# Optimization experiments

Hardware: AMD Instinct MI355X
Metric: run time of the kernel (lower is better)

## Reference

```python
import jax, jax.numpy as jnp
import numpy as np

N_NODES = 100000
N_CLIQUES = 50000
N_EDGES = 1600000
D_IN = 128
D_OUT = 128


def setup_inputs() -> dict:
    key = jax.random.key(0)
    k1, k2, k3, k4, k5, k6 = jax.random.split(key, 6)
    x = jax.random.normal(k1, (N_NODES, D_IN), dtype=jnp.float32)
    x_clique = jax.random.normal(k2, (N_CLIQUES, D_IN), dtype=jnp.float32)
    node_idx = jax.random.randint(k3, (N_EDGES,), 0, N_NODES, dtype=jnp.int64)
    clique_idx = jax.random.randint(k4, (N_EDGES,), 0, N_CLIQUES, dtype=jnp.int64)
    node2clique_index = jnp.stack([node_idx, clique_idx], axis=0)
    # Linear(in, out): weight [out, in], bias [out]
    W = jax.random.normal(k5, (D_OUT, D_IN), dtype=jnp.float32) * (1.0 / np.sqrt(D_IN))
    b = jax.random.normal(k6, (D_OUT,), dtype=jnp.float32) * 0.01
    return {"x": x, "x_clique": x_clique, "node2clique_index": node2clique_index, "W": W, "b": b}


def reference(x, x_clique, node2clique_index, W, b):
    node_idx = node2clique_index[0]
    clique_idx = node2clique_index[1]
    n_nodes = x.shape[0]
    gathered = x_clique[clique_idx]                                   # [E, D_in]
    summed = jax.ops.segment_sum(gathered, node_idx, num_segments=n_nodes)  # [N, D_in]
    count = jax.ops.segment_sum(
        jnp.ones((gathered.shape[0],), dtype=x_clique.dtype), node_idx, num_segments=n_nodes
    )
    mean = summed / jnp.maximum(count, 1.0)[:, None]                  # scatter-mean, count clamped like torch_scatter
    out = mean @ W.T + b                                              # Linear
    return out
```

## Files before the change

kernel.cpp:

```cpp
#include <hip/hip_runtime.h>


typedef short bf16x8 __attribute__((ext_vector_type(8)));
typedef float f32x4  __attribute__((ext_vector_type(4)));
typedef float f32x2  __attribute__((ext_vector_type(2)));

#define BK_SHIFT 8
#define NB_MAX 512
#define BCUR_STRIDE 16
#define RAWCAP 4608
#define PADCAP 6400
#define FCHUNK 4096

__device__ inline ushort f2b(float f) {
    union { float f; uint u; } v; v.f = f;
    uint r = v.u + 0x7FFFu + ((v.u >> 16) & 1u);
    return (ushort)(r >> 16);
}
__device__ inline float blo(uint v) { union { uint u; float f; } x; x.u = v << 16;        return x.f; }
__device__ inline float bhi(uint v) { union { uint u; float f; } x; x.u = v & 0xFFFF0000u; return x.f; }

struct FillSM {
    int cnt[NB_MAX];
    int sloc[NB_MAX];
    int gbase[NB_MAX];
    int cur[NB_MAX];
    int wtot[8];
    uint   stage[FCHUNK];
    ushort sbkt[FCHUNK];
};
struct TransSM { ushort wl[128 * 128]; };

__global__ __launch_bounds__(512) void k_front(const float* __restrict__ xc,
                                               const float* __restrict__ W,
                                               ushort* __restrict__ yb, int nc,
                                               const int* __restrict__ nidx,
                                               const int* __restrict__ cidx,
                                               int* __restrict__ bcur,
                                               uint* __restrict__ pairs,
                                               int ne, int gf) {
    __shared__ union USM { FillSM f; TransSM tr; } sm;
    const int t = threadIdx.x;
    const int lane = t & 63, wid = t >> 6;

    if ((int)blockIdx.x < gf) {
        const int e0 = blockIdx.x * FCHUNK;
        const int e1 = min(e0 + FCHUNK, ne);
        sm.f.cnt[t] = 0;
        sm.f.cur[t] = 0;
        __syncthreads();

        int nn[8], cc[8];
        #pragma unroll
        for (int k = 0; k < 8; ++k) {
            int i = e0 + k * 512 + t;
            if (i < e1) {
                nn[k] = nidx[i];
                cc[k] = cidx[i];
                atomicAdd(&sm.f.cnt[nn[k] >> BK_SHIFT], 1);
            } else nn[k] = -1;
        }
        __syncthreads();

        int v = sm.f.cnt[t];
        int inc = v;
        #pragma unroll
        for (int d = 1; d < 64; d <<= 1) { int x = __shfl_up(inc, d); if (lane >= d) inc += x; }
        if (lane == 63) sm.f.wtot[wid] = inc;
        __syncthreads();
        int wpre = 0;
        for (int i = 0; i < wid; ++i) wpre += sm.f.wtot[i];
        int excl = wpre + inc - v;
        sm.f.sloc[t] = excl;
        if (v > 0) sm.f.gbase[t] = t * RAWCAP + atomicAdd(&bcur[t * BCUR_STRIDE], v);
        __syncthreads();

        #pragma unroll
        for (int k = 0; k < 8; ++k) {
            if (nn[k] >= 0) {
                int b = nn[k] >> BK_SHIFT;
                int slot = sm.f.sloc[b] + atomicAdd(&sm.f.cur[b], 1);
                sm.f.stage[slot] = ((uint)(nn[k] & 255) << 16) | (uint)cc[k];
                sm.f.sbkt[slot] = (ushort)b;
            }
        }
        __syncthreads();

        const int m = e1 - e0;
        for (int i = t; i < m; i += 512) {
            int b = sm.f.sbkt[i];
            pairs[(size_t)sm.f.gbase[b] + (i - sm.f.sloc[b])] = sm.f.stage[i];
        }
    } else {
        const int bid = blockIdx.x - gf;
        if (bid == 0 && t < 64)
            reinterpret_cast<uint*>(&yb[(size_t)nc * 128])[t] = 0u;
        for (int i = 0; i < 8; ++i) {
            int idx = (i * 512 + t) * 4;
            float4 w4 = *reinterpret_cast<const float4*>(&W[idx]);
            int o = idx >> 7, k = idx & 127;
            ushort4 h;
            h.x = f2b(w4.x); h.y = f2b(w4.y); h.z = f2b(w4.z); h.w = f2b(w4.w);
            int byte = o * 256 + k * 2;
            byte ^= (o & 7) << 4;
            *reinterpret_cast<ushort4*>(reinterpret_cast<char*>(sm.tr.wl) + byte) = h;
        }
        __syncthreads();

        const int lrow = lane & 15;
        const int lk = lane >> 4;
        const int r0 = bid * 128 + wid * 16;
        const bool rowok = (r0 + lrow) < nc;
        const float* arow = &xc[(size_t)(r0 + lrow) * 128];

        bf16x8 afrag[4];
        for (int kb = 0; kb < 4; ++kb) {
            float4 a0 = make_float4(0.f, 0.f, 0.f, 0.f), a1 = a0;
            if (rowok) {
                int k0 = kb * 32 + lk * 8;
                a0 = *reinterpret_cast<const float4*>(&arow[k0]);
                a1 = *reinterpret_cast<const float4*>(&arow[k0 + 4]);
            }
            bf16x8 a;
            a[0] = (short)f2b(a0.x); a[1] = (short)f2b(a0.y);
            a[2] = (short)f2b(a0.z); a[3] = (short)f2b(a0.w);
            a[4] = (short)f2b(a1.x); a[5] = (short)f2b(a1.y);
            a[6] = (short)f2b(a1.z); a[7] = (short)f2b(a1.w);
            afrag[kb] = a;
        }

        for (int ct = 0; ct < 8; ++ct) {
            f32x4 c = {0.f, 0.f, 0.f, 0.f};
            const int o = ct * 16 + lrow;
            #pragma unroll
            for (int kb = 0; kb < 4; ++kb) {
                int byte = o * 256 + (kb * 32 + lk * 8) * 2;
                byte ^= (o & 7) << 4;
                bf16x8 bb = *reinterpret_cast<const bf16x8*>(reinterpret_cast<const char*>(sm.tr.wl) + byte);
                c = __builtin_amdgcn_mfma_f32_16x16x32_bf16(afrag[kb], bb, c, 0, 0, 0);
            }
            const int orow = r0 + lk * 4;
            #pragma unroll
            for (int j = 0; j < 4; ++j)
                if (orow + j < nc)
                    yb[(size_t)(orow + j) * 128 + ct * 16 + lrow] = f2b(c[j]);
        }
    }
}

__global__ __launch_bounds__(512) void k_build(const uint* __restrict__ pairs,
                                               const int* __restrict__ bcur,
                                               int* __restrict__ offsets,
                                               int* __restrict__ ncnt,
                                               ushort* __restrict__ edge_dst,
                                               int n_nodes, int nc) {
    __shared__ int arr[256], nexcl[256], cur[256], wtot[4];
    __shared__ int mpad_sh;
    __shared__ ushort scidx[PADCAP];
    const int b = blockIdx.x, t = threadIdx.x;
    const int p0r = b * RAWCAP;
    const int p0e = b * PADCAP;
    const int m = min(bcur[b * BCUR_STRIDE], RAWCAP);
    const int node0 = b << BK_SHIFT;

    if (t < 256) { arr[t] = 0; cur[t] = 0; }
    __syncthreads();
    for (int i = t; i < m; i += 512)
        atomicAdd(&arr[pairs[p0r + i] >> 16], 1);
    __syncthreads();

    int v = 0, pv = 0, inc = 0;
    if (t < 256) {
        v = arr[t];
        pv = (v + 7) & ~7;
        inc = pv;
        #pragma unroll
        for (int d = 1; d < 64; d <<= 1) {
            int x = __shfl_up(inc, d);
            if ((t & 63) >= d) inc += x;
        }
        if ((t & 63) == 63) wtot[t >> 6] = inc;
    }
    __syncthreads();
    if (t < 256) {
        const int wid = t >> 6;
        int wpre = 0;
        for (int i = 0; i < wid; ++i) wpre += wtot[i];
        const int excl = wpre + inc - pv;
        nexcl[t] = excl;
        if (node0 + t < n_nodes) {
            offsets[node0 + t] = p0e + excl;
            ncnt[node0 + t] = v;
        }
        if (t == 255) mpad_sh = excl + pv;
    }
    __syncthreads();

    for (int i = t; i < m; i += 512) {
        uint p = pairs[p0r + i];
        int l = (int)(p >> 16);
        int slot = nexcl[l] + atomicAdd(&cur[l], 1);
        scidx[slot] = (ushort)(p & 0xFFFFu);
    }
    __syncthreads();
    if (t < 256) {
        const int base = nexcl[t];
        for (int k = v; k < pv; ++k)
            scidx[base + k] = (ushort)nc;
    }
    __syncthreads();
    const int mp2 = mpad_sh >> 1;
    uint* ed32 = reinterpret_cast<uint*>(edge_dst);
    const uint* sc32 = reinterpret_cast<const uint*>(scidx);
    const int p0e2 = p0e >> 1;
    for (int i = t; i < mp2; i += 512)
        ed32[p0e2 + i] = sc32[i];
}

__global__ __launch_bounds__(256) void k_reduce(const ushort* __restrict__ yb,
                                                const int* __restrict__ offsets,
                                                const int* __restrict__ ncnt,
                                                const ushort* __restrict__ edge_dst,
                                                const float* __restrict__ bias,
                                                float* __restrict__ out, int n) {
    int w = (blockIdx.x * blockDim.x + threadIdx.x) >> 6;
    int nA = w << 1;
    if (nA >= n) return;
    const int lane = threadIdx.x & 63;
    const int nAu = __builtin_amdgcn_readfirstlane(nA);
    const int sA = offsets[nAu];
    const int cA = ncnt[nAu];
    const bool hasB = (nAu + 1) < n;
    const int sB = hasB ? offsets[nAu + 1] : sA;
    const int cB = hasB ? ncnt[nAu + 1] : 0;
    const int eA = (cA + 7) & ~7;
    const int eB = (cB + 7) & ~7;
    const char* ybase = reinterpret_cast<const char*>(yb) + lane * 4;

    float axA0 = 0.f, ayA0 = 0.f, axA1 = 0.f, ayA1 = 0.f;
    float axB0 = 0.f, ayB0 = 0.f, axB1 = 0.f, ayB1 = 0.f;
    const int rounds = (max(eA, eB) + 7) >> 3;
    for (int r = 0; r < rounds; ++r) {
        const int j = r << 3;
        const bool doA = j < eA, doB = j < eB;
        uint vA[8], vB[8];
        if (doA) {
            #pragma unroll
            for (int u = 0; u < 8; ++u) {
                int c = edge_dst[sA + j + u];
                vA[u] = *reinterpret_cast<const uint*>(ybase + (size_t)c * 256);
            }
        }
        if (doB) {
            #pragma unroll
            for (int u = 0; u < 8; ++u) {
                int c = edge_dst[sB + j + u];
                vB[u] = *reinterpret_cast<const uint*>(ybase + (size_t)c * 256);
            }
        }
        if (doA) {
            #pragma unroll
            for (int u = 0; u < 8; u += 2) {
                axA0 += blo(vA[u]);     ayA0 += bhi(vA[u]);
                axA1 += blo(vA[u + 1]); ayA1 += bhi(vA[u + 1]);
            }
        }
        if (doB) {
            #pragma unroll
            for (int u = 0; u < 8; u += 2) {
                axB0 += blo(vB[u]);     ayB0 += bhi(vB[u]);
                axB1 += blo(vB[u + 1]); ayB1 += bhi(vB[u + 1]);
            }
        }
    }
    const f32x2 bv = *reinterpret_cast<const f32x2*>(&bias[lane * 2]);
    {
        float ax = axA0 + axA1, ay = ayA0 + ayA1;
        float inv = 1.0f / (float)max(cA, 1);
        f32x2 o;
        o.x = ax * inv + bv.x;
        o.y = ay * inv + bv.y;
        __builtin_nontemporal_store(o, reinterpret_cast<f32x2*>(&out[(size_t)nA * 128 + lane * 2]));
    }
    if (hasB) {
        float ax = axB0 + axB1, ay = ayB0 + ayB1;
        float inv = 1.0f / (float)max(cB, 1);
        f32x2 o;
        o.x = ax * inv + bv.x;
        o.y = ay * inv + bv.y;
        __builtin_nontemporal_store(o, reinterpret_cast<f32x2*>(&out[((size_t)nA + 1) * 128 + lane * 2]));
    }
}

extern "C" void kernel_launch(void* const* d_in, const int* in_sizes, int n_in,
                              void* d_out, int out_size, void* d_ws, size_t ws_size,
                              hipStream_t stream) {
    const float* xc  = (const float*)d_in[1];
    const int*   n2c = (const int*)d_in[2];
    const float* W   = (const float*)d_in[3];
    const float* b   = (const float*)d_in[4];
    float* out = (float*)d_out;

    const int n_nodes   = in_sizes[0] / 128;
    const int n_cliques = in_sizes[1] / 128;
    const int n_edges   = in_sizes[2] / 2;
    const int* nidx = n2c;
    const int* cidx = n2c + n_edges;
    const int nbucket = (n_nodes + ((1 << BK_SHIFT) - 1)) >> BK_SHIFT;

    char* ws = (char*)d_ws;
    size_t off = 0;
    ushort* yb = (ushort*)(ws + off);     off += (size_t)(n_cliques + 1) * 128 * sizeof(ushort);
    off = (off + 15) & ~(size_t)15;
    uint* pairs = (uint*)(ws + off);      off += (size_t)nbucket * RAWCAP * sizeof(uint);
    ushort* edge_dst = (ushort*)(ws + off); off += (size_t)nbucket * PADCAP * sizeof(ushort);
    off = (off + 15) & ~(size_t)15;
    int* offsets = (int*)(ws + off);      off += (size_t)n_nodes * sizeof(int);
    int* ncnt = (int*)(ws + off);         off += (size_t)n_nodes * sizeof(int);
    int* bcur = (int*)(ws + off);         off += (size_t)NB_MAX * BCUR_STRIDE * sizeof(int);

    (void)hipMemsetAsync(bcur, 0, (size_t)NB_MAX * BCUR_STRIDE * sizeof(int), stream);

    const int gf = (n_edges + FCHUNK - 1) / FCHUNK;
    const int gt = (n_cliques + 127) / 128;
    k_front<<<gf + gt, 512, 0, stream>>>(xc, W, yb, n_cliques, nidx, cidx, bcur,
                                         pairs, n_edges, gf);
    k_build<<<nbucket, 512, 0, stream>>>(pairs, bcur, offsets, ncnt, edge_dst,
                                         n_nodes, n_cliques);
    const int nwaves = (n_nodes + 1) / 2;
    k_reduce<<<(nwaves * 64 + 255) / 256, 256, 0, stream>>>(yb, offsets, ncnt, edge_dst, b, out, n_nodes);
}
```

Baseline: 96.27 us.

## Reduce one node per wave with 16-byte gathers across four edge groups

The reduce kernel now gives each wave one node instead of two. The wave is split into four groups of 16 lanes; each group handles every fourth edge and each lane gathers 16 bytes (8 bf16 values) of a projected clique row. Partial sums are combined with cross-lane shuffles, and only 16 lanes write the output row. This aims for wider gather loads and more edges in flight per wave, at the cost of shuffle reductions and idle lanes during the final write. Separately, the transform blocks in the front kernel each process 256 clique rows instead of 128, so the W load into shared memory is spread over more rows.

```diff
diff --git a/kernel.cpp b/kernel.cpp
--- a/kernel.cpp
+++ b/kernel.cpp
@@ -109,41 +109,43 @@
 
         const int lrow = lane & 15;
         const int lk = lane >> 4;
-        const int r0 = bid * 128 + wid * 16;
-        const bool rowok = (r0 + lrow) < nc;
-        const float* arow = &xc[(size_t)(r0 + lrow) * 128];
-
-        bf16x8 afrag[4];
-        for (int kb = 0; kb < 4; ++kb) {
-            float4 a0 = make_float4(0.f, 0.f, 0.f, 0.f), a1 = a0;
-            if (rowok) {
-                int k0 = kb * 32 + lk * 8;
-                a0 = *reinterpret_cast<const float4*>(&arow[k0]);
-                a1 = *reinterpret_cast<const float4*>(&arow[k0 + 4]);
+        for (int g = 0; g < 2; ++g) {
+            const int r0 = bid * 256 + g * 128 + wid * 16;
+            const bool rowok = (r0 + lrow) < nc;
+            const float* arow = &xc[(size_t)(r0 + lrow) * 128];
+
+            bf16x8 afrag[4];
+            for (int kb = 0; kb < 4; ++kb) {
+                float4 a0 = make_float4(0.f, 0.f, 0.f, 0.f), a1 = a0;
+                if (rowok) {
+                    int k0 = kb * 32 + lk * 8;
+                    a0 = *reinterpret_cast<const float4*>(&arow[k0]);
+                    a1 = *reinterpret_cast<const float4*>(&arow[k0 + 4]);
+                }
+                bf16x8 a;
+                a[0] = (short)f2b(a0.x); a[1] = (short)f2b(a0.y);
+                a[2] = (short)f2b(a0.z); a[3] = (short)f2b(a0.w);
+                a[4] = (short)f2b(a1.x); a[5] = (short)f2b(a1.y);
+                a[6] = (short)f2b(a1.z); a[7] = (short)f2b(a1.w);
+                afrag[kb] = a;
             }
-            bf16x8 a;
-            a[0] = (short)f2b(a0.x); a[1] = (short)f2b(a0.y);
-            a[2] = (short)f2b(a0.z); a[3] = (short)f2b(a0.w);
-            a[4] = (short)f2b(a1.x); a[5] = (short)f2b(a1.y);
-            a[6] = (short)f2b(a1.z); a[7] = (short)f2b(a1.w);
-            afrag[kb] = a;
-        }
-
-        for (int ct = 0; ct < 8; ++ct) {
-            f32x4 c = {0.f, 0.f, 0.f, 0.f};
-            const int o = ct * 16 + lrow;
-            #pragma unroll
-            for (int kb = 0; kb < 4; ++kb) {
-                int byte = o * 256 + (kb * 32 + lk * 8) * 2;
-                byte ^= (o & 7) << 4;
-                bf16x8 bb = *reinterpret_cast<const bf16x8*>(reinterpret_cast<const char*>(sm.tr.wl) + byte);
-                c = __builtin_amdgcn_mfma_f32_16x16x32_bf16(afrag[kb], bb, c, 0, 0, 0);
+
+            for (int ct = 0; ct < 8; ++ct) {
+                f32x4 c = {0.f, 0.f, 0.f, 0.f};
+                const int o = ct * 16 + lrow;
+                #pragma unroll
+                for (int kb = 0; kb < 4; ++kb) {
+                    int byte = o * 256 + (kb * 32 + lk * 8) * 2;
+                    byte ^= (o & 7) << 4;
+                    bf16x8 bb = *reinterpret_cast<const bf16x8*>(reinterpret_cast<const char*>(sm.tr.wl) + byte);
+                    c = __builtin_amdgcn_mfma_f32_16x16x32_bf16(afrag[kb], bb, c, 0, 0, 0);
+                }
+                const int orow = r0 + lk * 4;
+                #pragma unroll
+                for (int j = 0; j < 4; ++j)
+                    if (orow + j < nc)
+                        yb[(size_t)(orow + j) * 128 + ct * 16 + lrow] = f2b(c[j]);
             }
-            const int orow = r0 + lk * 4;
-            #pragma unroll
-            for (int j = 0; j < 4; ++j)
-                if (orow + j < nc)
-                    yb[(size_t)(orow + j) * 128 + ct * 16 + lrow] = f2b(c[j]);
         }
     }
 }
@@ -223,72 +225,55 @@
                                                 const ushort* __restrict__ edge_dst,
                                                 const float* __restrict__ bias,
                                                 float* __restrict__ out, int n) {
-    int w = (blockIdx.x * blockDim.x + threadIdx.x) >> 6;
-    int nA = w << 1;
-    if (nA >= n) return;
+    int gw = (blockIdx.x * blockDim.x + threadIdx.x) >> 6;
+    if (gw >= n) return;
     const int lane = threadIdx.x & 63;
-    const int nAu = __builtin_amdgcn_readfirstlane(nA);
-    const int sA = offsets[nAu];
-    const int cA = ncnt[nAu];
-    const bool hasB = (nAu + 1) < n;
-    const int sB = hasB ? offsets[nAu + 1] : sA;
-    const int cB = hasB ? ncnt[nAu + 1] : 0;
-    const int eA = (cA + 7) & ~7;
-    const int eB = (cB + 7) & ~7;
-    const char* ybase = reinterpret_cast<const char*>(yb) + lane * 4;
-
-    float axA0 = 0.f, ayA0 = 0.f, axA1 = 0.f, ayA1 = 0.f;
-    float axB0 = 0.f, ayB0 = 0.f, axB1 = 0.f, ayB1 = 0.f;
-    const int rounds = (max(eA, eB) + 7) >> 3;
+    const int eg = lane >> 4;
+    const int ch = lane & 15;
+    const int gwu = __builtin_amdgcn_readfirstlane(gw);
+    const int s = offsets[gwu];
+    const int cnt = ncnt[gwu];
+    const int rounds = ((cnt + 7) & ~7) >> 2;
+
+    const ushort* ep = edge_dst + s + eg;
+    const char* ybase = reinterpret_cast<const char*>(yb) + ch * 16;
+
+    float a0 = 0.f, a1 = 0.f, a2 = 0.f, a3 = 0.f;
+    float a4 = 0.f, a5 = 0.f, a6 = 0.f, a7 = 0.f;
+    #pragma unroll 2
     for (int r = 0; r < rounds; ++r) {
-        const int j = r << 3;
-        const bool doA = j < eA, doB = j < eB;
-        uint vA[8], vB[8];
-        if (doA) {
-            #pragma unroll
-            for (int u = 0; u < 8; ++u) {
-                int c = edge_dst[sA + j + u];
-                vA[u] = *reinterpret_cast<const uint*>(ybase + (size_t)c * 256);
-            }
-        }
-        if (doB) {
-            #pragma unroll
-            for (int u = 0; u < 8; ++u) {
-                int c = edge_dst[sB + j + u];
-                vB[u] = *reinterpret_cast<const uint*>(ybase + (size_t)c * 256);
-            }
-        }
-        if (doA) {
-            #pragma unroll
-            for (int u = 0; u < 8; u += 2) {
-                axA0 += blo(vA[u]);     ayA0 += bhi(vA[u]);
-                axA1 += blo(vA[u + 1]); ayA1 += bhi(vA[u + 1]);
-            }
-        }
-        if (doB) {
-            #pragma unroll
-            for (int u = 0; u < 8; u += 2) {
-                axB0 += blo(vB[u]);     ayB0 += bhi(vB[u]);
-                axB1 += blo(vB[u + 1]); ayB1 += bhi(vB[u + 1]);
-            }
-        }
-    }
-    const f32x2 bv = *reinterpret_cast<const f32x2*>(&bias[lane * 2]);
-    {
-        float ax = axA0 + axA1, ay = ayA0 + ayA1;
-        float inv = 1.0f / (float)max(cA, 1);
-        f32x2 o;
-        o.x = ax * inv + bv.x;
-        o.y = ay * inv + bv.y;
-        __builtin_nontemporal_store(o, reinterpret_cast<f32x2*>(&out[(size_t)nA * 128 + lane * 2]));
-    }
-    if (hasB) {
-        float ax = axB0 + axB1, ay = ayB0 + ayB1;
-        float inv = 1.0f / (float)max(cB, 1);
-        f32x2 o;
-        o.x = ax * inv + bv.x;
-        o.y = ay * inv + bv.y;
-        __builtin_nontemporal_store(o, reinterpret_cast<f32x2*>(&out[((size_t)nA + 1) * 128 + lane * 2]));
+        uint c = ep[r * 4];
+        uint4 v = *reinterpret_cast<const uint4*>(ybase + (size_t)c * 256);
+        a0 += blo(v.x); a1 += bhi(v.x);
+        a2 += blo(v.y); a3 += bhi(v.y);
+        a4 += blo(v.z); a5 += bhi(v.z);
+        a6 += blo(v.w); a7 += bhi(v.w);
+    }
+    a0 += __shfl_xor(a0, 16); a0 += __shfl_xor(a0, 32);
+    a1 += __shfl_xor(a1, 16); a1 += __shfl_xor(a1, 32);
+    a2 += __shfl_xor(a2, 16); a2 += __shfl_xor(a2, 32);
+    a3 += __shfl_xor(a3, 16); a3 += __shfl_xor(a3, 32);
+    a4 += __shfl_xor(a4, 16); a4 += __shfl_xor(a4, 32);
+    a5 += __shfl_xor(a5, 16); a5 += __shfl_xor(a5, 32);
+    a6 += __shfl_xor(a6, 16); a6 += __shfl_xor(a6, 32);
+    a7 += __shfl_xor(a7, 16); a7 += __shfl_xor(a7, 32);
+
+    if (lane < 16) {
+        const float inv = 1.0f / (float)max(cnt, 1);
+        const f32x4 bv0 = *reinterpret_cast<const f32x4*>(&bias[ch * 8]);
+        const f32x4 bv1 = *reinterpret_cast<const f32x4*>(&bias[ch * 8 + 4]);
+        f32x4 o0, o1;
+        o0.x = a0 * inv + bv0.x;
+        o0.y = a1 * inv + bv0.y;
+        o0.z = a2 * inv + bv0.z;
+        o0.w = a3 * inv + bv0.w;
+        o1.x = a4 * inv + bv1.x;
+        o1.y = a5 * inv + bv1.y;
+        o1.z = a6 * inv + bv1.z;
+        o1.w = a7 * inv + bv1.w;
+        float* orow = &out[(size_t)gw * 128 + ch * 8];
+        __builtin_nontemporal_store(o0, reinterpret_cast<f32x4*>(orow));
+        __builtin_nontemporal_store(o1, reinterpret_cast<f32x4*>(orow + 4));
     }
 }
 
@@ -322,11 +307,10 @@
     (void)hipMemsetAsync(bcur, 0, (size_t)NB_MAX * BCUR_STRIDE * sizeof(int), stream);
 
     const int gf = (n_edges + FCHUNK - 1) / FCHUNK;
-    const int gt = (n_cliques + 127) / 128;
+    const int gt = (n_cliques + 255) / 256;
     k_front<<<gf + gt, 512, 0, stream>>>(xc, W, yb, n_cliques, nidx, cidx, bcur,
                                          pairs, n_edges, gf);
     k_build<<<nbucket, 512, 0, stream>>>(pairs, bcur, offsets, ncnt, edge_dst,
                                          n_nodes, n_cliques);
-    const int nwaves = (n_nodes + 1) / 2;
-    k_reduce<<<(nwaves * 64 + 255) / 256, 256, 0, stream>>>(yb, offsets, ncnt, edge_dst, b, out, n_nodes);
-}
+    k_reduce<<<((n_nodes) * 64 + 255) / 256, 256, 0, stream>>>(yb, offsets, ncnt, edge_dst, b, out, n_nodes);
+}
```

Result: slower. 104.6 us (+8.7%).
